# Kernel tuning notes

Measured on AMD Instinct MI355X. Metric: run time of the kernel, lower is better.

Reference implementation:

```python
import jax, jax.numpy as jnp
import numpy as np

B, N, D = 2, 2048, 1024
H = 16
HD = D // H  # 64
ROPE_BASE = 10000.0


def setup_inputs() -> dict:
    key = jax.random.key(0)
    ks = jax.random.split(key, 5)
    s = 0.02
    return {
        "x": jax.random.normal(ks[0], (B, N, D), dtype=jnp.float32),
        "qkv_w": jax.random.normal(ks[1], (3 * D, D), dtype=jnp.float32) * s,
        "qkv_b": jax.random.normal(ks[2], (3 * D,), dtype=jnp.float32) * s,
        "proj_w": jax.random.normal(ks[3], (D, D), dtype=jnp.float32) * s,
        "proj_b": jax.random.normal(ks[4], (D,), dtype=jnp.float32) * s,
    }


def _rotate_half(t):
    # interleaved pairs: (x1,x2) -> (-x2,x1), matching lucidrains RotaryEmbedding
    t = t.reshape(*t.shape[:-1], -1, 2)
    x1, x2 = t[..., 0], t[..., 1]
    return jnp.stack((-x2, x1), axis=-1).reshape(*t.shape[:-2], -1)


def _apply_rope(t, cos, sin):
    # t: [B, H, N, HD]; cos/sin: [N, HD]
    return t * cos + _rotate_half(t) * sin


def reference(x, qkv_w, qkv_b, proj_w, proj_b):
    b, n, d = x.shape
    scale = HD ** -0.5

    qkv = x @ qkv_w.T + qkv_b                      # [B, N, 3D]
    qkv = qkv.reshape(b, n, 3, H, HD)
    qkv = jnp.transpose(qkv, (2, 0, 3, 1, 4))       # [3, B, H, N, HD]
    q, k, v = qkv[0], qkv[1], qkv[2]

    # RoPE (lang freqs, interpolate_factor=1)
    inv_freq = 1.0 / (ROPE_BASE ** (jnp.arange(0, HD, 2, dtype=jnp.float32) / HD))
    freqs = jnp.arange(n, dtype=jnp.float32)[:, None] * inv_freq[None, :]  # [N, HD/2]
    freqs = jnp.repeat(freqs, 2, axis=-1)           # [N, HD] interleaved
    cos, sin = jnp.cos(freqs), jnp.sin(freqs)
    q = _apply_rope(q, cos, sin)
    k = _apply_rope(k, cos, sin)

    scores = jnp.einsum('bhid,bhjd->bhij', q, k) * scale  # [B, H, N, N]
    causal = jnp.triu(jnp.ones((n, n), dtype=bool), k=1)
    scores = jnp.where(causal, -jnp.inf, scores)
    attn = jax.nn.softmax(scores, axis=-1)

    out = jnp.einsum('bhij,bhjd->bhid', attn, v)    # [B, H, N, HD]
    out = jnp.transpose(out, (0, 2, 1, 3)).reshape(b, n, d)
    return out @ proj_w.T + proj_b
```

## Files before the change

kernel.cpp:

```cpp
#include <hip/hip_runtime.h>
#include <hip/hip_bf16.h>
#include <cstdint>
#include <cstddef>

typedef __hip_bfloat16 bf16;
typedef short bf16x8 __attribute__((ext_vector_type(8)));
typedef float f32x4 __attribute__((ext_vector_type(4)));
typedef int i32x4 __attribute__((ext_vector_type(4)));

#define MFMA16(a, b, c) __builtin_amdgcn_mfma_f32_16x16x32_bf16((a), (b), (c), 0, 0, 0)

__device__ __forceinline__ void glds16(const bf16* g, bf16* l)
{
    __builtin_amdgcn_global_load_lds(
        (const __attribute__((address_space(1))) void*)g,
        (__attribute__((address_space(3))) void*)l, 16, 0, 0);
}

__global__ void cvt_f32_bf16(const float* __restrict__ in, bf16* __restrict__ out, int n4)
{
    int i = blockIdx.x * blockDim.x + threadIdx.x;
    if (i >= n4) return;
    float4 v = *reinterpret_cast<const float4*>(in + (size_t)i * 4);
    __align__(8) bf16 tmp[4];
    tmp[0] = __float2bfloat16(v.x);
    tmp[1] = __float2bfloat16(v.y);
    tmp[2] = __float2bfloat16(v.z);
    tmp[3] = __float2bfloat16(v.w);
    *reinterpret_cast<short4*>(out + (size_t)i * 4) = *reinterpret_cast<short4*>(tmp);
}

__global__ void rope_table_kernel(float2* __restrict__ tab)
{
    int i = blockIdx.x * blockDim.x + threadIdx.x;
    int pos = i >> 5, f = i & 31;
    float inv = powf(10000.f, -(float)f * (1.f / 32.f));
    float ang = (float)pos * inv;
    tab[i] = make_float2(cosf(ang), sinf(ang));
}

__global__ void rope_apply_kernel(bf16* __restrict__ qkv, const float2* __restrict__ tab)
{
    int idx = blockIdx.x * blockDim.x + threadIdx.x;
    int row = idx >> 8;
    int cc  = (idx & 255) * 8;
    int pos = row & 2047;
    int hd  = cc & 63;
    bf16* p = qkv + (size_t)row * 3072 + cc;
    i32x4 v = *reinterpret_cast<const i32x4*>(p);
    bf16* e = reinterpret_cast<bf16*>(&v);
    const float2* tb = tab + pos * 32 + (hd >> 1);
#pragma unroll
    for (int pp = 0; pp < 4; ++pp) {
        float2 cs = tb[pp];
        float x1 = __bfloat162float(e[2 * pp]);
        float x2 = __bfloat162float(e[2 * pp + 1]);
        e[2 * pp]     = __float2bfloat16(x1 * cs.x - x2 * cs.y);
        e[2 * pp + 1] = __float2bfloat16(x2 * cs.x + x1 * cs.y);
    }
    *reinterpret_cast<i32x4*>(p) = v;
}

__device__ inline void store_out(float* p, float v) { *p = v; }
__device__ inline void store_out(bf16* p, float v) { *p = __float2bfloat16(v); }

template <typename OutT>
__global__ void gemm_bt_kernel(const bf16* __restrict__ A, const bf16* __restrict__ BT,
                               const float* __restrict__ bias, OutT* __restrict__ C,
                               int M, int N, int K)
{
    constexpr int BM = 128, BN = 128, BK = 32;
    __shared__ __align__(16) bf16 Al[BM * BK];
    __shared__ __align__(16) bf16 Bl[BN * BK];

    const int tid = threadIdx.x;
    const int l = tid & 63;
    const int w = tid >> 6;
    const int wr = w >> 1, wc = w & 1;
    const int l15 = l & 15, lhi = l >> 4;
    const int row0 = blockIdx.x * BM, col0 = blockIdx.y * BN;

    const int ar0 = tid >> 2, ar1 = (tid + 256) >> 2;
    const int ac  = (tid & 3) * 8;
    const bf16* Ag0 = A + (size_t)(row0 + ar0) * K + ac;
    const bf16* Ag1 = A + (size_t)(row0 + ar1) * K + ac;
    const bf16* Bg0 = BT + (size_t)(col0 + ar0) * K + ac;
    const bf16* Bg1 = BT + (size_t)(col0 + ar1) * K + ac;
    const int wbase = (tid & 192) * 8;
    bf16* sA0 = &Al[wbase];
    bf16* sA1 = &Al[2048 + wbase];
    bf16* sB0 = &Bl[wbase];
    bf16* sB1 = &Bl[2048 + wbase];

    f32x4 acc[4][4] = {};

    for (int k0 = 0; k0 < K; k0 += BK) {
        __syncthreads();
        glds16(Ag0 + k0, sA0);
        glds16(Ag1 + k0, sA1);
        glds16(Bg0 + k0, sB0);
        glds16(Bg1 + k0, sB1);
        __syncthreads();
        bf16x8 af[4], bfr[4];
#pragma unroll
        for (int m = 0; m < 4; ++m)
            af[m] = *reinterpret_cast<const bf16x8*>(&Al[(wr * 64 + m * 16 + l15) * BK + lhi * 8]);
#pragma unroll
        for (int n = 0; n < 4; ++n)
            bfr[n] = *reinterpret_cast<const bf16x8*>(&Bl[(wc * 64 + n * 16 + l15) * BK + lhi * 8]);
#pragma unroll
        for (int m = 0; m < 4; ++m)
#pragma unroll
            for (int n = 0; n < 4; ++n)
                acc[m][n] = MFMA16(af[m], bfr[n], acc[m][n]);
    }

#pragma unroll
    for (int m = 0; m < 4; ++m) {
#pragma unroll
        for (int n = 0; n < 4; ++n) {
            int col = col0 + wc * 64 + n * 16 + l15;
            float bs = bias[col];
#pragma unroll
            for (int j = 0; j < 4; ++j) {
                int row = row0 + wr * 64 + m * 16 + lhi * 4 + j;
                store_out(&C[(size_t)row * N + col], acc[m][n][j] + bs);
            }
        }
    }
}

__global__ void attn_kernel(const bf16* __restrict__ qkv, bf16* __restrict__ outp)
{
    constexpr int LDK = 72;
    __shared__ __align__(16) bf16 Kl[64 * LDK];
    __shared__ __align__(16) bf16 Vt[64 * LDK];
    __shared__ __align__(16) bf16 Pl[64 * LDK];

    const int bh = blockIdx.x;
    const int b = bh >> 4, h = bh & 15;
    const int q0 = (31 - blockIdx.y) * 64;
    const int tid = threadIdx.x;
    const int w = tid >> 6, l = tid & 63;
    const int lane15 = l & 15, lhi = l >> 4;

    const size_t RS = 3072;
    const bf16* base = qkv + (size_t)b * 2048 * RS;

    bf16x8 qf0, qf1;
    {
        const bf16* qr = base + (size_t)(q0 + w * 16 + lane15) * RS + h * 64 + lhi * 8;
        qf0 = *reinterpret_cast<const bf16x8*>(qr);
        qf1 = *reinterpret_cast<const bf16x8*>(qr + 32);
    }

    float m_run[4], l_run[4];
    f32x4 o_acc[4] = {};
#pragma unroll
    for (int j = 0; j < 4; ++j) { m_run[j] = -1e30f; l_run[j] = 0.f; }

    const int ntiles = q0 / 64 + 1;
    for (int t = 0; t < ntiles; ++t) {
        const int kv0 = t * 64;
        __syncthreads();
#pragma unroll
        for (int cc = 0; cc < 2; ++cc) {
            int c = tid + cc * 256;
            int r = c >> 3, c8 = (c & 7) * 8;
            i32x4 v = *reinterpret_cast<const i32x4*>(base + (size_t)(kv0 + r) * RS + 1024 + h * 64 + c8);
            *reinterpret_cast<i32x4*>(&Kl[r * LDK + c8]) = v;
        }
        {
            const int hd = l;
            const int seg = w;
            const bf16* vcol = base + (size_t)(kv0 + seg * 16) * RS + 2048 + h * 64 + hd;
            __align__(16) bf16 tmp[16];
#pragma unroll
            for (int j = 0; j < 16; ++j) tmp[j] = vcol[(size_t)j * RS];
            *reinterpret_cast<i32x4*>(&Vt[hd * LDK + seg * 16])     = *reinterpret_cast<const i32x4*>(&tmp[0]);
            *reinterpret_cast<i32x4*>(&Vt[hd * LDK + seg * 16 + 8]) = *reinterpret_cast<const i32x4*>(&tmp[8]);
        }
        __syncthreads();

        f32x4 s[4] = {};
#pragma unroll
        for (int n = 0; n < 4; ++n) {
            bf16x8 kf0 = *reinterpret_cast<const bf16x8*>(&Kl[(n * 16 + lane15) * LDK + lhi * 8]);
            bf16x8 kf1 = *reinterpret_cast<const bf16x8*>(&Kl[(n * 16 + lane15) * LDK + 32 + lhi * 8]);
            s[n] = MFMA16(qf0, kf0, s[n]);
            s[n] = MFMA16(qf1, kf1, s[n]);
        }

        const int qrow = q0 + w * 16 + lhi * 4;
#pragma unroll
        for (int n = 0; n < 4; ++n) {
            const int kvc = kv0 + n * 16 + lane15;
#pragma unroll
            for (int j = 0; j < 4; ++j) {
                float v = s[n][j] * 0.125f;
                s[n][j] = (kvc > qrow + j) ? -1e30f : v;
            }
        }

        float alpha[4];
#pragma unroll
        for (int j = 0; j < 4; ++j) {
            float rm = fmaxf(fmaxf(s[0][j], s[1][j]), fmaxf(s[2][j], s[3][j]));
            rm = fmaxf(rm, __shfl_xor(rm, 1));
            rm = fmaxf(rm, __shfl_xor(rm, 2));
            rm = fmaxf(rm, __shfl_xor(rm, 4));
            rm = fmaxf(rm, __shfl_xor(rm, 8));
            float mnew = fmaxf(m_run[j], rm);
            alpha[j] = __expf(m_run[j] - mnew);
            m_run[j] = mnew;
        }
        float rs[4] = {0.f, 0.f, 0.f, 0.f};
#pragma unroll
        for (int n = 0; n < 4; ++n)
#pragma unroll
            for (int j = 0; j < 4; ++j) {
                float p = __expf(s[n][j] - m_run[j]);
                s[n][j] = p;
                rs[j] += p;
            }
#pragma unroll
        for (int j = 0; j < 4; ++j) {
            float r = rs[j];
            r += __shfl_xor(r, 1);
            r += __shfl_xor(r, 2);
            r += __shfl_xor(r, 4);
            r += __shfl_xor(r, 8);
            l_run[j] = l_run[j] * alpha[j] + r;
            o_acc[0][j] *= alpha[j];
            o_acc[1][j] *= alpha[j];
            o_acc[2][j] *= alpha[j];
            o_acc[3][j] *= alpha[j];
        }

        bf16* Pw = &Pl[w * 16 * LDK];
#pragma unroll
        for (int n = 0; n < 4; ++n)
#pragma unroll
            for (int j = 0; j < 4; ++j)
                Pw[(lhi * 4 + j) * LDK + n * 16 + lane15] = __float2bfloat16(s[n][j]);

        bf16x8 pa0 = *reinterpret_cast<const bf16x8*>(&Pw[lane15 * LDK + lhi * 8]);
        bf16x8 pa1 = *reinterpret_cast<const bf16x8*>(&Pw[lane15 * LDK + 32 + lhi * 8]);
#pragma unroll
        for (int t2 = 0; t2 < 4; ++t2) {
            bf16x8 vf0 = *reinterpret_cast<const bf16x8*>(&Vt[(t2 * 16 + lane15) * LDK + lhi * 8]);
            bf16x8 vf1 = *reinterpret_cast<const bf16x8*>(&Vt[(t2 * 16 + lane15) * LDK + 32 + lhi * 8]);
            o_acc[t2] = MFMA16(pa0, vf0, o_acc[t2]);
            o_acc[t2] = MFMA16(pa1, vf1, o_acc[t2]);
        }
    }

#pragma unroll
    for (int j = 0; j < 4; ++j) {
        float inv = 1.f / l_run[j];
        size_t row = (size_t)(b * 2048 + q0 + w * 16 + lhi * 4 + j);
#pragma unroll
        for (int t2 = 0; t2 < 4; ++t2)
            outp[row * 1024 + h * 64 + t2 * 16 + lane15] = __float2bfloat16(o_acc[t2][j] * inv);
    }
}

extern "C" void kernel_launch(void* const* d_in, const int* in_sizes, int n_in,
                              void* d_out, int out_size, void* d_ws, size_t ws_size,
                              hipStream_t stream)
{
    const float* x      = (const float*)d_in[0];
    const float* qkv_w  = (const float*)d_in[1];
    const float* qkv_b  = (const float*)d_in[2];
    const float* proj_w = (const float*)d_in[3];
    const float* proj_b = (const float*)d_in[4];
    float* out = (float*)d_out;

    char* ws = (char*)d_ws;
    bf16* x_bf   = (bf16*)ws;  ws += (size_t)4096 * 1024 * 2;
    bf16* wq_bf  = (bf16*)ws;  ws += (size_t)3072 * 1024 * 2;
    bf16* wp_bf  = (bf16*)ws;  ws += (size_t)1024 * 1024 * 2;
    bf16* qkvbuf = (bf16*)ws;  ws += (size_t)4096 * 3072 * 2;
    bf16* aout   = (bf16*)ws;  ws += (size_t)4096 * 1024 * 2;
    float2* tab  = (float2*)ws;

    cvt_f32_bf16<<<4096, 256, 0, stream>>>(x, x_bf, 1048576);
    cvt_f32_bf16<<<3072, 256, 0, stream>>>(qkv_w, wq_bf, 786432);
    cvt_f32_bf16<<<1024, 256, 0, stream>>>(proj_w, wp_bf, 262144);
    rope_table_kernel<<<256, 256, 0, stream>>>(tab);

    gemm_bt_kernel<bf16><<<dim3(32, 24), 256, 0, stream>>>(x_bf, wq_bf, qkv_b, qkvbuf, 4096, 3072, 1024);
    rope_apply_kernel<<<4096, 256, 0, stream>>>(qkvbuf, tab);
    attn_kernel<<<dim3(32, 32), 256, 0, stream>>>(qkvbuf, aout);
    gemm_bt_kernel<float><<<dim3(32, 8), 256, 0, stream>>>(aout, wp_bf, proj_b, out, 4096, 1024, 1024);
}
```

Measured before the change: 220.5 us.

## Double-buffer K/V tiles in attention with register prefetch of next tile

The attention kernel now keeps two LDS buffers for K and transposed V. It issues the global loads for the next KV tile into registers before computing on the current tile, then writes them to the alternate buffer after the PV MFMAs. This cuts the syncs per iteration from two to one and hides global load latency behind compute. In exchange it doubles K/V LDS use and raises register pressure from holding the prefetched tile.

```diff
diff --git a/kernel.cpp b/kernel.cpp
--- a/kernel.cpp
+++ b/kernel.cpp
@@ -133,8 +133,8 @@
 __global__ void attn_kernel(const bf16* __restrict__ qkv, bf16* __restrict__ outp)
 {
     constexpr int LDK = 72;
-    __shared__ __align__(16) bf16 Kl[64 * LDK];
-    __shared__ __align__(16) bf16 Vt[64 * LDK];
+    __shared__ __align__(16) bf16 Kl[2][64 * LDK];
+    __shared__ __align__(16) bf16 Vt[2][64 * LDK];
     __shared__ __align__(16) bf16 Pl[64 * LDK];
 
     const int bh = blockIdx.x;
@@ -142,51 +142,63 @@
     const int q0 = (31 - blockIdx.y) * 64;
     const int tid = threadIdx.x;
     const int w = tid >> 6, l = tid & 63;
-    const int lane15 = l & 15, lhi = l >> 4;
+    const int l15 = l & 15, lhi = l >> 4;
 
     const size_t RS = 3072;
     const bf16* base = qkv + (size_t)b * 2048 * RS;
 
     bf16x8 qf0, qf1;
     {
-        const bf16* qr = base + (size_t)(q0 + w * 16 + lane15) * RS + h * 64 + lhi * 8;
+        const bf16* qr = base + (size_t)(q0 + w * 16 + l15) * RS + h * 64 + lhi * 8;
         qf0 = *reinterpret_cast<const bf16x8*>(qr);
         qf1 = *reinterpret_cast<const bf16x8*>(qr + 32);
     }
 
+    const int kr  = tid >> 3;
+    const int kc8 = (tid & 7) * 8;
+    const bf16* kp = base + (size_t)kr * RS + 1024 + h * 64 + kc8;
+    const bf16* vp = base + (size_t)(w * 16) * RS + 2048 + h * 64 + l;
+
+    i32x4 ka, kb;
+    __align__(16) bf16 vt16[16];
+
+    ka = *reinterpret_cast<const i32x4*>(kp);
+    kb = *reinterpret_cast<const i32x4*>(kp + 32 * RS);
+#pragma unroll
+    for (int j = 0; j < 16; ++j) vt16[j] = vp[(size_t)j * RS];
+    *reinterpret_cast<i32x4*>(&Kl[0][kr * LDK + kc8])        = ka;
+    *reinterpret_cast<i32x4*>(&Kl[0][(kr + 32) * LDK + kc8]) = kb;
+    *reinterpret_cast<i32x4*>(&Vt[0][l * LDK + w * 16])      = *reinterpret_cast<const i32x4*>(&vt16[0]);
+    *reinterpret_cast<i32x4*>(&Vt[0][l * LDK + w * 16 + 8])  = *reinterpret_cast<const i32x4*>(&vt16[8]);
+    __syncthreads();
+
     float m_run[4], l_run[4];
     f32x4 o_acc[4] = {};
 #pragma unroll
     for (int j = 0; j < 4; ++j) { m_run[j] = -1e30f; l_run[j] = 0.f; }
 
     const int ntiles = q0 / 64 + 1;
+    int cur = 0;
     for (int t = 0; t < ntiles; ++t) {
         const int kv0 = t * 64;
-        __syncthreads();
-#pragma unroll
-        for (int cc = 0; cc < 2; ++cc) {
-            int c = tid + cc * 256;
-            int r = c >> 3, c8 = (c & 7) * 8;
-            i32x4 v = *reinterpret_cast<const i32x4*>(base + (size_t)(kv0 + r) * RS + 1024 + h * 64 + c8);
-            *reinterpret_cast<i32x4*>(&Kl[r * LDK + c8]) = v;
-        }
-        {
-            const int hd = l;
-            const int seg = w;
-            const bf16* vcol = base + (size_t)(kv0 + seg * 16) * RS + 2048 + h * 64 + hd;
-            __align__(16) bf16 tmp[16];
-#pragma unroll
-            for (int j = 0; j < 16; ++j) tmp[j] = vcol[(size_t)j * RS];
-            *reinterpret_cast<i32x4*>(&Vt[hd * LDK + seg * 16])     = *reinterpret_cast<const i32x4*>(&tmp[0]);
-            *reinterpret_cast<i32x4*>(&Vt[hd * LDK + seg * 16 + 8]) = *reinterpret_cast<const i32x4*>(&tmp[8]);
-        }
-        __syncthreads();
+        const bool pf = (t + 1 < ntiles);
+        if (pf) {
+            kp += 64 * RS;
+            vp += 64 * RS;
+            ka = *reinterpret_cast<const i32x4*>(kp);
+            kb = *reinterpret_cast<const i32x4*>(kp + 32 * RS);
+#pragma unroll
+            for (int j = 0; j < 16; ++j) vt16[j] = vp[(size_t)j * RS];
+        }
+
+        const bf16* Kc = &Kl[cur][0];
+        const bf16* Vc = &Vt[cur][0];
 
         f32x4 s[4] = {};
 #pragma unroll
         for (int n = 0; n < 4; ++n) {
-            bf16x8 kf0 = *reinterpret_cast<const bf16x8*>(&Kl[(n * 16 + lane15) * LDK + lhi * 8]);
-            bf16x8 kf1 = *reinterpret_cast<const bf16x8*>(&Kl[(n * 16 + lane15) * LDK + 32 + lhi * 8]);
+            bf16x8 kf0 = *reinterpret_cast<const bf16x8*>(&Kc[(n * 16 + l15) * LDK + lhi * 8]);
+            bf16x8 kf1 = *reinterpret_cast<const bf16x8*>(&Kc[(n * 16 + l15) * LDK + 32 + lhi * 8]);
             s[n] = MFMA16(qf0, kf0, s[n]);
             s[n] = MFMA16(qf1, kf1, s[n]);
         }
@@ -194,7 +206,7 @@
         const int qrow = q0 + w * 16 + lhi * 4;
 #pragma unroll
         for (int n = 0; n < 4; ++n) {
-            const int kvc = kv0 + n * 16 + lane15;
+            const int kvc = kv0 + n * 16 + l15;
 #pragma unroll
             for (int j = 0; j < 4; ++j) {
                 float v = s[n][j] * 0.125f;
@@ -242,16 +254,26 @@
         for (int n = 0; n < 4; ++n)
 #pragma unroll
             for (int j = 0; j < 4; ++j)
-                Pw[(lhi * 4 + j) * LDK + n * 16 + lane15] = __float2bfloat16(s[n][j]);
-
-        bf16x8 pa0 = *reinterpret_cast<const bf16x8*>(&Pw[lane15 * LDK + lhi * 8]);
-        bf16x8 pa1 = *reinterpret_cast<const bf16x8*>(&Pw[lane15 * LDK + 32 + lhi * 8]);
+                Pw[(lhi * 4 + j) * LDK + n * 16 + l15] = __float2bfloat16(s[n][j]);
+
+        bf16x8 pa0 = *reinterpret_cast<const bf16x8*>(&Pw[l15 * LDK + lhi * 8]);
+        bf16x8 pa1 = *reinterpret_cast<const bf16x8*>(&Pw[l15 * LDK + 32 + lhi * 8]);
 #pragma unroll
         for (int t2 = 0; t2 < 4; ++t2) {
-            bf16x8 vf0 = *reinterpret_cast<const bf16x8*>(&Vt[(t2 * 16 + lane15) * LDK + lhi * 8]);
-            bf16x8 vf1 = *reinterpret_cast<const bf16x8*>(&Vt[(t2 * 16 + lane15) * LDK + 32 + lhi * 8]);
+            bf16x8 vf0 = *reinterpret_cast<const bf16x8*>(&Vc[(t2 * 16 + l15) * LDK + lhi * 8]);
+            bf16x8 vf1 = *reinterpret_cast<const bf16x8*>(&Vc[(t2 * 16 + l15) * LDK + 32 + lhi * 8]);
             o_acc[t2] = MFMA16(pa0, vf0, o_acc[t2]);
             o_acc[t2] = MFMA16(pa1, vf1, o_acc[t2]);
+        }
+
+        if (pf) {
+            const int nxt = cur ^ 1;
+            *reinterpret_cast<i32x4*>(&Kl[nxt][kr * LDK + kc8])        = ka;
+            *reinterpret_cast<i32x4*>(&Kl[nxt][(kr + 32) * LDK + kc8]) = kb;
+            *reinterpret_cast<i32x4*>(&Vt[nxt][l * LDK + w * 16])      = *reinterpret_cast<const i32x4*>(&vt16[0]);
+            *reinterpret_cast<i32x4*>(&Vt[nxt][l * LDK + w * 16 + 8])  = *reinterpret_cast<const i32x4*>(&vt16[8]);
+            __syncthreads();
+            cur = nxt;
         }
     }
 
@@ -261,7 +283,7 @@
         size_t row = (size_t)(b * 2048 + q0 + w * 16 + lhi * 4 + j);
 #pragma unroll
         for (int t2 = 0; t2 < 4; ++t2)
-            outp[row * 1024 + h * 64 + t2 * 16 + lane15] = __float2bfloat16(o_acc[t2][j] * inv);
+            outp[row * 1024 + h * 64 + t2 * 16 + l15] = __float2bfloat16(o_acc[t2][j] * inv);
     }
 }
 
```

Result: no change. 218.6 us (-0.9%).
